# Kernel optimization log

Hardware: AMD Instinct MI355X
Metric: run time of the kernel (lower is better)

## Reference

```python
import jax, jax.numpy as jnp
import numpy as np

TEMPERATURE = 0.5
EPS = 1e-8  # matches torch cosine_similarity eps guard semantics (norm clamp)


def setup_inputs() -> dict:
    key = jax.random.key(0)
    k1, k2 = jax.random.split(key)
    B, D = 4096, 256
    z_i = jax.random.normal(k1, (B, D), dtype=jnp.float32)
    z_j = jax.random.normal(k2, (B, D), dtype=jnp.float32)
    return {"z_i": z_i, "z_j": z_j}


def reference(z_i, z_j):
    B = z_i.shape[0]
    z = jnp.concatenate([z_i, z_j], axis=0)            # [2B, D]
    # cosine similarity: normalize once, then GEMM
    norm = jnp.maximum(jnp.linalg.norm(z, axis=1, keepdims=True), EPS)
    zn = z / norm                                       # [2B, D]
    sim = zn @ zn.T                                     # [2B, 2B]
    # positives: diag(sim, +B) and diag(sim, -B)
    idx = jnp.arange(B)
    sim_ij = sim[idx, idx + B]
    sim_ji = sim[idx + B, idx]
    positives = jnp.concatenate([sim_ij, sim_ji])       # [2B]
    # masked denominator: exclude self-similarity
    mask = 1.0 - jnp.eye(2 * B, dtype=sim.dtype)
    denom = jnp.sum(mask * jnp.exp(sim / TEMPERATURE), axis=1)  # [2B]
    all_losses = -jnp.log(jnp.exp(positives / TEMPERATURE) / denom)
    return jnp.sum(all_losses) / (2 * B)
```

## Files before the change

kernel.cpp:

```cpp
#include <hip/hip_runtime.h>
#include <hip/hip_bf16.h>
#include <cstdint>
#include <cstddef>
#include <math.h>

#define D 256
#define TEMP_INV 2.0f
#define EPS_NORM 1e-8f
#define NTILES 2080

typedef __attribute__((ext_vector_type(8))) short bf16x8;
typedef __attribute__((ext_vector_type(4))) float f32x4;

#define GLOAD16(g, l)                                                   \
  __builtin_amdgcn_global_load_lds(                                     \
      (const __attribute__((address_space(1))) void*)(g),               \
      (__attribute__((address_space(3))) void*)(l), 16, 0, 0)

__global__ void __launch_bounds__(256) normalize_rows(
    const float* __restrict__ zi, const float* __restrict__ zj,
    __hip_bfloat16* __restrict__ zn, float* __restrict__ out, int B) {
  const int wid = threadIdx.x >> 6;
  const int lane = threadIdx.x & 63;
  if (blockIdx.x == 0 && threadIdx.x == 0) out[0] = 0.0f;
#pragma unroll
  for (int it = 0; it < 4; ++it) {
    int row = it * 2048 + blockIdx.x * 4 + wid;
    const float* src = (row < B) ? (zi + (size_t)row * D)
                                 : (zj + (size_t)(row - B) * D);
    float4 v = ((const float4*)src)[lane];
    float ss = v.x * v.x + v.y * v.y + v.z * v.z + v.w * v.w;
    for (int off = 32; off; off >>= 1) ss += __shfl_xor(ss, off);
    float rn = 1.0f / fmaxf(sqrtf(ss), EPS_NORM);
    union { ushort4 u; __hip_bfloat16 h[4]; } o;
    o.h[0] = __float2bfloat16(v.x * rn);
    o.h[1] = __float2bfloat16(v.y * rn);
    o.h[2] = __float2bfloat16(v.z * rn);
    o.h[3] = __float2bfloat16(v.w * rn);
    ((ushort4*)zn)[(size_t)row * (D / 4) + lane] = o.u;
  }
}

__device__ __forceinline__ void decode_tile(int t, int Nb, int& by, int& bx) {
  float fb = (2.0f * Nb + 1.0f -
              sqrtf((float)((2 * Nb + 1) * (2 * Nb + 1) - 8 * t))) * 0.5f;
  int y = (int)fb;
  while ((y + 1) * Nb - ((y + 1) * y) / 2 <= t) ++y;
  while (y * Nb - (y * (y - 1)) / 2 > t) --y;
  by = y;
  bx = y + (t - (y * Nb - (y * (y - 1)) / 2));
}

__global__ void __launch_bounds__(256, 2) ntxent_gemm(
    const __hip_bfloat16* __restrict__ zn,
    float* __restrict__ part, float* __restrict__ pos, int B) {
  __shared__ __align__(16) __hip_bfloat16 Ash[2][128 * 64];
  __shared__ __align__(16) __hip_bfloat16 Bsh[2][128 * 64];

  const int N = 2 * B;
  const int Nb = N / 128;
  int by, bx;
  decode_tile(blockIdx.x, Nb, by, bx);
  const int bm = by * 128;
  const int bn = bx * 128;
  const bool isDiag = (by == bx);
  const bool isPos = (bx == by + B / 128);

  const int tid = threadIdx.x;
  const int wid = tid >> 6;
  const int lane = tid & 63;
  const int wy = wid >> 1, wx = wid & 1;
  const int wrow0 = wid * 32;

  const int lr = lane >> 3;
  const int c8 = lane & 7;

  const int frow = lane & 15;
  const int quad = lane >> 4;
  const int f7 = frow & 7;

  f32x4 acc[4][4] = {};

  const __hip_bfloat16* gA =
      zn + (size_t)(bm + wrow0 + lr) * D + (c8 ^ lr) * 8;
  const __hip_bfloat16* gB =
      zn + (size_t)(bn + wrow0 + lr) * D + (c8 ^ lr) * 8;

#pragma unroll
  for (int s = 0; s < 4; ++s) {
    GLOAD16(gA + s * 8 * D, &Ash[0][(wrow0 + s * 8) * 64]);
    GLOAD16(gB + s * 8 * D, &Bsh[0][(wrow0 + s * 8) * 64]);
  }
  __syncthreads();

#pragma unroll
  for (int k0i = 0; k0i < 4; ++k0i) {
    const int cur = k0i & 1;
    if (k0i < 3) {
      const int k0 = (k0i + 1) * 64;
#pragma unroll
      for (int s = 0; s < 4; ++s) {
        GLOAD16(gA + s * 8 * D + k0, &Ash[cur ^ 1][(wrow0 + s * 8) * 64]);
        GLOAD16(gB + s * 8 * D + k0, &Bsh[cur ^ 1][(wrow0 + s * 8) * 64]);
      }
    }
#pragma unroll
    for (int kk = 0; kk < 2; ++kk) {
      bf16x8 a[4], b[4];
#pragma unroll
      for (int i = 0; i < 4; ++i)
        a[i] = *(const bf16x8*)
            &Ash[cur][(wy * 64 + i * 16 + frow) * 64 + ((kk * 4 + quad) ^ f7) * 8];
#pragma unroll
      for (int j = 0; j < 4; ++j)
        b[j] = *(const bf16x8*)
            &Bsh[cur][(wx * 64 + j * 16 + frow) * 64 + ((kk * 4 + quad) ^ f7) * 8];
#pragma unroll
      for (int i = 0; i < 4; ++i)
#pragma unroll
        for (int j = 0; j < 4; ++j)
          acc[i][j] =
              __builtin_amdgcn_mfma_f32_16x16x32_bf16(a[i], b[j], acc[i][j], 0, 0, 0);
    }
    __syncthreads();
  }

  float* red = (float*)&Ash[0][0];

  const int colq = lane & 15;
  float cs[4] = {0.0f, 0.0f, 0.0f, 0.0f};
#pragma unroll
  for (int i = 0; i < 4; ++i) {
#pragma unroll
    for (int r = 0; r < 4; ++r) {
      int rowloc = wy * 64 + i * 16 + quad * 4 + r;
      int row = bm + rowloc;
      float rs = 0.0f;
#pragma unroll
      for (int j = 0; j < 4; ++j) {
        int col = bn + wx * 64 + j * 16 + colq;
        float v = acc[i][j][r];
        float e = __expf(v * TEMP_INV);
        e = (isDiag && col == row) ? 0.0f : e;
        rs += e;
        cs[j] += e;
        if (isPos && col == row + B) { pos[row] = v; pos[col] = v; }
      }
      rs += __shfl_xor(rs, 1);
      rs += __shfl_xor(rs, 2);
      rs += __shfl_xor(rs, 4);
      rs += __shfl_xor(rs, 8);
      if (colq == 0) red[rowloc * 2 + wx] = rs;
    }
  }
#pragma unroll
  for (int j = 0; j < 4; ++j) {
    float c = cs[j];
    c += __shfl_xor(c, 16);
    c += __shfl_xor(c, 32);
    if (quad == 0) red[256 + (wx * 64 + j * 16 + colq) * 2 + wy] = c;
  }
  __syncthreads();
  if (tid < 128) {
    part[(size_t)bx * N + bm + tid] = red[tid * 2] + red[tid * 2 + 1];
  } else if (!isDiag) {
    int t = tid - 128;
    part[(size_t)by * N + bn + t] = red[256 + t * 2] + red[256 + t * 2 + 1];
  }
}

__global__ void __launch_bounds__(256) finalize(
    const float* __restrict__ part, const float* __restrict__ pos,
    float* __restrict__ out, int N) {
  const int idx = blockIdx.x * 256 + threadIdx.x;
  const int NS = N / 128;
  float s = 0.0f;
#pragma unroll 8
  for (int k = 0; k < NS; ++k) s += part[(size_t)k * N + idx];
  float loss = __logf(s) - pos[idx] * TEMP_INV;
  for (int off = 32; off; off >>= 1) loss += __shfl_xor(loss, off);
  __shared__ float redsh[4];
  if ((threadIdx.x & 63) == 0) redsh[threadIdx.x >> 6] = loss;
  __syncthreads();
  if (threadIdx.x == 0) {
    float t = redsh[0] + redsh[1] + redsh[2] + redsh[3];
    atomicAdd(out, t / (float)N);
  }
}

extern "C" void kernel_launch(void* const* d_in, const int* in_sizes, int n_in,
                              void* d_out, int out_size, void* d_ws, size_t ws_size,
                              hipStream_t stream) {
  const float* zi = (const float*)d_in[0];
  const float* zj = (const float*)d_in[1];
  const int B = in_sizes[0] / D;
  const int N = 2 * B;

  __hip_bfloat16* zn = (__hip_bfloat16*)d_ws;
  float* pos = (float*)((char*)d_ws + (size_t)N * D * sizeof(__hip_bfloat16));
  float* part = pos + N;

  normalize_rows<<<512, 256, 0, stream>>>(zi, zj, zn, (float*)d_out, B);
  ntxent_gemm<<<NTILES, 256, 0, stream>>>(zn, part, pos, B);
  finalize<<<N / 256, 256, 0, stream>>>(part, pos, (float*)d_out, N);
}
```

Measured before the change: 115.5 us.

## Hold A fragments in registers and stage full-K B tile in LDS

Each wave now loads its 32 rows of A straight from global memory into registers as MFMA fragments for the whole K=256. The full 128x256 B tile is staged into LDS once, which drops the double-buffered K loop and its per-iteration barriers. Waves are rearranged into a 4x1 layout (32 rows by 128 columns each), so row sums are written straight to global memory without an LDS reduction. The cost is more register pressure (16 A fragments plus 16 accumulators) and uncoalesced fragment-shaped global loads for A. LDS use per block stays at 64KB.

```diff
diff --git a/kernel.cpp b/kernel.cpp
--- a/kernel.cpp
+++ b/kernel.cpp
@@ -54,8 +54,7 @@
 __global__ void __launch_bounds__(256, 2) ntxent_gemm(
     const __hip_bfloat16* __restrict__ zn,
     float* __restrict__ part, float* __restrict__ pos, int B) {
-  __shared__ __align__(16) __hip_bfloat16 Ash[2][128 * 64];
-  __shared__ __align__(16) __hip_bfloat16 Bsh[2][128 * 64];
+  __shared__ __align__(16) __hip_bfloat16 Bsh[4][128 * 64];
 
   const int N = 2 * B;
   const int Nb = N / 128;
@@ -67,79 +66,64 @@
   const bool isPos = (bx == by + B / 128);
 
   const int tid = threadIdx.x;
-  const int wid = tid >> 6;
+  const int w = tid >> 6;
   const int lane = tid & 63;
-  const int wy = wid >> 1, wx = wid & 1;
-  const int wrow0 = wid * 32;
-
+  const int frow = lane & 15;
+  const int quad = lane >> 4;
+  const int f7 = frow & 7;
   const int lr = lane >> 3;
   const int c8 = lane & 7;
 
-  const int frow = lane & 15;
-  const int quad = lane >> 4;
-  const int f7 = frow & 7;
+  const __hip_bfloat16* gB =
+      zn + (size_t)(bn + w * 32 + lr) * D + (c8 ^ lr) * 8;
+#pragma unroll
+  for (int kb = 0; kb < 4; ++kb)
+#pragma unroll
+    for (int s = 0; s < 4; ++s)
+      GLOAD16(gB + (size_t)s * 8 * D + kb * 64,
+              &Bsh[kb][(w * 32 + s * 8) * 64]);
 
-  f32x4 acc[4][4] = {};
+  bf16x8 aF[2][8];
+  const __hip_bfloat16* gA =
+      zn + (size_t)(bm + w * 32 + frow) * D + quad * 8;
+#pragma unroll
+  for (int m = 0; m < 2; ++m)
+#pragma unroll
+    for (int kc = 0; kc < 8; ++kc)
+      aF[m][kc] = *(const bf16x8*)(gA + (size_t)m * 16 * D + kc * 32);
 
-  const __hip_bfloat16* gA =
-      zn + (size_t)(bm + wrow0 + lr) * D + (c8 ^ lr) * 8;
-  const __hip_bfloat16* gB =
-      zn + (size_t)(bn + wrow0 + lr) * D + (c8 ^ lr) * 8;
-
-#pragma unroll
-  for (int s = 0; s < 4; ++s) {
-    GLOAD16(gA + s * 8 * D, &Ash[0][(wrow0 + s * 8) * 64]);
-    GLOAD16(gB + s * 8 * D, &Bsh[0][(wrow0 + s * 8) * 64]);
-  }
   __syncthreads();
 
+  f32x4 acc[2][8] = {};
 #pragma unroll
-  for (int k0i = 0; k0i < 4; ++k0i) {
-    const int cur = k0i & 1;
-    if (k0i < 3) {
-      const int k0 = (k0i + 1) * 64;
+  for (int kc = 0; kc < 8; ++kc) {
+    const int kb = kc >> 1, kk = kc & 1;
+    bf16x8 b[8];
 #pragma unroll
-      for (int s = 0; s < 4; ++s) {
-        GLOAD16(gA + s * 8 * D + k0, &Ash[cur ^ 1][(wrow0 + s * 8) * 64]);
-        GLOAD16(gB + s * 8 * D + k0, &Bsh[cur ^ 1][(wrow0 + s * 8) * 64]);
-      }
+    for (int j = 0; j < 8; ++j)
+      b[j] = *(const bf16x8*)
+          &Bsh[kb][(j * 16 + frow) * 64 + ((kk * 4 + quad) ^ f7) * 8];
+#pragma unroll
+    for (int j = 0; j < 8; ++j) {
+      acc[0][j] = __builtin_amdgcn_mfma_f32_16x16x32_bf16(aF[0][kc], b[j],
+                                                          acc[0][j], 0, 0, 0);
+      acc[1][j] = __builtin_amdgcn_mfma_f32_16x16x32_bf16(aF[1][kc], b[j],
+                                                          acc[1][j], 0, 0, 0);
     }
-#pragma unroll
-    for (int kk = 0; kk < 2; ++kk) {
-      bf16x8 a[4], b[4];
-#pragma unroll
-      for (int i = 0; i < 4; ++i)
-        a[i] = *(const bf16x8*)
-            &Ash[cur][(wy * 64 + i * 16 + frow) * 64 + ((kk * 4 + quad) ^ f7) * 8];
-#pragma unroll
-      for (int j = 0; j < 4; ++j)
-        b[j] = *(const bf16x8*)
-            &Bsh[cur][(wx * 64 + j * 16 + frow) * 64 + ((kk * 4 + quad) ^ f7) * 8];
-#pragma unroll
-      for (int i = 0; i < 4; ++i)
-#pragma unroll
-        for (int j = 0; j < 4; ++j)
-          acc[i][j] =
-              __builtin_amdgcn_mfma_f32_16x16x32_bf16(a[i], b[j], acc[i][j], 0, 0, 0);
-    }
-    __syncthreads();
   }
 
-  float* red = (float*)&Ash[0][0];
-
-  const int colq = lane & 15;
-  float cs[4] = {0.0f, 0.0f, 0.0f, 0.0f};
+  const int colq = frow;
+  float cs[8] = {};
 #pragma unroll
-  for (int i = 0; i < 4; ++i) {
+  for (int m = 0; m < 2; ++m) {
 #pragma unroll
     for (int r = 0; r < 4; ++r) {
-      int rowloc = wy * 64 + i * 16 + quad * 4 + r;
-      int row = bm + rowloc;
+      int row = bm + w * 32 + m * 16 + quad * 4 + r;
       float rs = 0.0f;
 #pragma unroll
-      for (int j = 0; j < 4; ++j) {
-        int col = bn + wx * 64 + j * 16 + colq;
-        float v = acc[i][j][r];
+      for (int j = 0; j < 8; ++j) {
+        int col = bn + j * 16 + colq;
+        float v = acc[m][j][r];
         float e = __expf(v * TEMP_INV);
         e = (isDiag && col == row) ? 0.0f : e;
         rs += e;
@@ -150,22 +134,22 @@
       rs += __shfl_xor(rs, 2);
       rs += __shfl_xor(rs, 4);
       rs += __shfl_xor(rs, 8);
-      if (colq == 0) red[rowloc * 2 + wx] = rs;
+      if (colq == 0) part[(size_t)bx * N + row] = rs;
     }
   }
+  float* colbuf = (float*)&Bsh[0][0];
+  __syncthreads();
 #pragma unroll
-  for (int j = 0; j < 4; ++j) {
+  for (int j = 0; j < 8; ++j) {
     float c = cs[j];
     c += __shfl_xor(c, 16);
     c += __shfl_xor(c, 32);
-    if (quad == 0) red[256 + (wx * 64 + j * 16 + colq) * 2 + wy] = c;
+    if (quad == 0) colbuf[(j * 16 + colq) * 4 + w] = c;
   }
   __syncthreads();
-  if (tid < 128) {
-    part[(size_t)bx * N + bm + tid] = red[tid * 2] + red[tid * 2 + 1];
-  } else if (!isDiag) {
-    int t = tid - 128;
-    part[(size_t)by * N + bn + t] = red[256 + t * 2] + red[256 + t * 2 + 1];
+  if (!isDiag && tid < 128) {
+    part[(size_t)by * N + bn + tid] = colbuf[tid * 4 + 0] + colbuf[tid * 4 + 1] +
+                                      colbuf[tid * 4 + 2] + colbuf[tid * 4 + 3];
   }
 }
 
```

Measured after the change: 115.3 us. No clear change (-0.1%).
